# Performance work log

Hardware: AMD Instinct MI355X
Metric: run time of the kernel (lower is better)

## Reference

```python
import jax, jax.numpy as jnp
import numpy as np


def setup_inputs() -> dict:
    key = jax.random.key(0)
    k1, k2 = jax.random.split(key)
    B, Lq, Lc, D = 16, 512, 2048, 1024
    question = jax.random.normal(k1, (B, Lq, D), dtype=jnp.float32)
    context = jax.random.normal(k2, (B, Lc, D), dtype=jnp.float32)
    return {"question": question, "context": context}


def reference(question, context):
    # e = context @ question^T : [B, Lc, Lq]  (unscaled)
    e = jnp.einsum("bcd,bqd->bcq", context, question)
    attn = jax.nn.softmax(e, axis=-1)
    # attention_output = attn @ question : [B, Lc, D]
    attn_out = jnp.einsum("bcq,bqd->bcd", attn, question)
    # concat along feature dim -> [B, Lc, 2D]; dropout is identity at eval
    return jnp.concatenate([context, attn_out], axis=-1)
```

## Files before the change

kernel.cpp:

```cpp
#include <hip/hip_runtime.h>

#define GAS __attribute__((address_space(1)))
#define LAS __attribute__((address_space(3)))

typedef __attribute__((ext_vector_type(8))) _Float16 half8;
typedef __attribute__((ext_vector_type(4))) float floatx4;
typedef __attribute__((ext_vector_type(4))) unsigned short ushort4v;

static constexpr int B_  = 16;
static constexpr int LQ  = 512;
static constexpr int LC  = 2048;
static constexpr int D_  = 1024;
static constexpr int DO  = 2048;
static constexpr int MT  = 64;
static constexpr int BUFSZ = 36864;

__device__ __forceinline__ void gl2lds16(const void* g, void* l) {
  __builtin_amdgcn_global_load_lds((const GAS unsigned int*)g,
                                   (LAS unsigned int*)l, 16, 0, 0);
}

__device__ __forceinline__ unsigned short f2h(float f) {
  return __builtin_bit_cast(unsigned short, (_Float16)f);
}

#define WAITV(a, b)                                                        \
  do {                                                                     \
    if (wave < 4) asm volatile("s_waitcnt vmcnt(" #a ")" ::: "memory");    \
    else          asm volatile("s_waitcnt vmcnt(" #b ")" ::: "memory");    \
  } while (0)

__global__ void qprep_kernel(const float* __restrict__ q,
                             unsigned short* __restrict__ qh,
                             unsigned short* __restrict__ qt) {
  __shared__ unsigned short t[32][33];
  const int b = blockIdx.z, d0 = blockIdx.x * 32, q0 = blockIdx.y * 32;
  const float* src = q + (size_t)b * LQ * D_;
  unsigned short* dq = qh + (size_t)b * LQ * D_;
  unsigned short* dt = qt + (size_t)b * D_ * LQ;
  for (int i = threadIdx.y; i < 32; i += 8) {
    const unsigned short h = f2h(src[(size_t)(q0 + i) * D_ + d0 + threadIdx.x]);
    dq[(size_t)(q0 + i) * D_ + d0 + threadIdx.x] = h;
    t[i][threadIdx.x] = h;
  }
  __syncthreads();
  for (int i = threadIdx.y; i < 32; i += 8)
    dt[(size_t)(d0 + i) * LQ + q0 + threadIdx.x] = t[threadIdx.x][i];
}

__global__ void cprep_kernel(const float* __restrict__ src,
                             unsigned short* __restrict__ dst,
                             float* __restrict__ out) {
  const int nrows = B_ * LC;
  for (int row = blockIdx.x; row < nrows; row += gridDim.x) {
    const float4 v = ((const float4*)(src + (size_t)row * D_))[threadIdx.x];
    ushort4v h;
    h.x = f2h(v.x); h.y = f2h(v.y); h.z = f2h(v.z); h.w = f2h(v.w);
    ((ushort4v*)(dst + (size_t)row * D_))[threadIdx.x] = h;
    ((float4*)(out + (size_t)row * DO))[threadIdx.x] = v;
  }
}

__launch_bounds__(512, 1)
__global__ void attn_main(const unsigned short* __restrict__ qg,
                          const unsigned short* __restrict__ cg,
                          const unsigned short* __restrict__ qtg,
                          unsigned short* __restrict__ pg,
                          float* __restrict__ og) {
  __shared__ __align__(16) char smem[4 * BUFSZ + 2048 + 256];
  float* redf    = (float*)(smem + 4 * BUFSZ);
  float* rowstat = (float*)(smem + 4 * BUFSZ + 2048);

  const int tid  = threadIdx.x;
  const int wave = tid >> 6;
  const int lane = tid & 63;
  const int l15  = lane & 15;
  const int quad = lane >> 4;
  const int q8   = quad * 8;

  const int b    = blockIdx.x & 15;
  const int tile = blockIdx.x >> 4;
  const int c0   = tile * MT;

  const unsigned short* Q  = qg  + (size_t)b * LQ * D_;
  const unsigned short* C  = cg  + (size_t)b * LC * D_;
  const unsigned short* QT = qtg + (size_t)b * D_ * LQ;
  unsigned short*       P  = pg  + (size_t)b * LC * LQ;
  float*                O  = og  + (size_t)b * LC * DO;

  floatx4 acc[4][4];

  auto stage1 = [&](int it, char* buf) {
    const int k0 = it * 32;
#pragma unroll
    for (int j = 0; j < 5; ++j) {
      const int bb = wave + j * 8;
      if (bb < 32) {
        gl2lds16(Q + (size_t)(bb * 16 + l15) * D_ + k0 + q8, buf + bb * 1024);
      } else if (bb < 36) {
        const int mt = bb - 32;
        gl2lds16(C + (size_t)(c0 + mt * 16 + l15) * D_ + k0 + q8,
                 buf + 32768 + mt * 1024);
      }
    }
  };

  auto stage2 = [&](int u, char* buf) {
    const int nh = u >> 4;
    const int kq = (u & 15) * 32;
#pragma unroll
    for (int j = 0; j < 5; ++j) {
      const int bb = wave + j * 8;
      if (bb < 32) {
        gl2lds16(QT + (size_t)(nh * 512 + bb * 16 + l15) * LQ + kq + q8,
                 buf + bb * 1024);
      } else if (bb < 36) {
        const int mt = bb - 32;
        gl2lds16(P + (size_t)(c0 + mt * 16 + l15) * LQ + kq + q8,
                 buf + 32768 + mt * 1024);
      }
    }
  };

  auto compute = [&](const char* buf) {
    half8 af[4], bf[4];
#pragma unroll
    for (int mt = 0; mt < 4; ++mt)
      af[mt] = *(const half8*)(buf + 32768 + mt * 1024 + lane * 16);
#pragma unroll
    for (int nt = 0; nt < 4; ++nt)
      bf[nt] = *(const half8*)(buf + (wave * 4 + nt) * 1024 + lane * 16);
    __builtin_amdgcn_s_setprio(1);
#pragma unroll
    for (int mt = 0; mt < 4; ++mt)
#pragma unroll
      for (int nt = 0; nt < 4; ++nt)
        acc[mt][nt] = __builtin_amdgcn_mfma_f32_16x16x32_f16(
            af[mt], bf[nt], acc[mt][nt], 0, 0, 0);
    __builtin_amdgcn_s_setprio(0);
  };

#pragma unroll
  for (int i = 0; i < 4; ++i)
#pragma unroll
    for (int j = 0; j < 4; ++j) acc[i][j] = floatx4{0.f, 0.f, 0.f, 0.f};

  stage1(0, smem);
  stage1(1, smem + BUFSZ);
  stage1(2, smem + 2 * BUFSZ);
#pragma unroll 1
  for (int t = 0; t < 32; ++t) {
    if (t <= 29)      WAITV(10, 8);
    else if (t == 30) WAITV(5, 4);
    else asm volatile("s_waitcnt vmcnt(0)" ::: "memory");
    __builtin_amdgcn_s_barrier();
    __builtin_amdgcn_sched_barrier(0);
    if (t + 3 < 32) stage1(t + 3, smem + ((t + 3) & 3) * BUFSZ);
    compute(smem + (t & 3) * BUFSZ);
    asm volatile("" ::: "memory");
    __builtin_amdgcn_s_barrier();
  }

#pragma unroll
  for (int mt = 0; mt < 4; ++mt)
#pragma unroll
    for (int r = 0; r < 4; ++r) {
      float m = fmaxf(fmaxf(acc[mt][0][r], acc[mt][1][r]),
                      fmaxf(acc[mt][2][r], acc[mt][3][r]));
      m = fmaxf(m, __shfl_xor(m, 1, 64));
      m = fmaxf(m, __shfl_xor(m, 2, 64));
      m = fmaxf(m, __shfl_xor(m, 4, 64));
      m = fmaxf(m, __shfl_xor(m, 8, 64));
      if (l15 == 0) redf[wave * 64 + mt * 16 + quad * 4 + r] = m;
    }
  __syncthreads();
  if (tid < 64) {
    float m = redf[tid];
#pragma unroll
    for (int w = 1; w < 8; ++w) m = fmaxf(m, redf[w * 64 + tid]);
    rowstat[tid] = m;
  }
  __syncthreads();
#pragma unroll
  for (int mt = 0; mt < 4; ++mt)
#pragma unroll
    for (int r = 0; r < 4; ++r) {
      const float m = rowstat[mt * 16 + quad * 4 + r];
      float s = 0.f;
#pragma unroll
      for (int nt = 0; nt < 4; ++nt) {
        const float e = __expf(acc[mt][nt][r] - m);
        acc[mt][nt][r] = e;
        s += e;
      }
      s += __shfl_xor(s, 1, 64);
      s += __shfl_xor(s, 2, 64);
      s += __shfl_xor(s, 4, 64);
      s += __shfl_xor(s, 8, 64);
      if (l15 == 0) redf[wave * 64 + mt * 16 + quad * 4 + r] = s;
    }
  __syncthreads();
  if (tid < 64) {
    float s = 0.f;
#pragma unroll
    for (int w = 0; w < 8; ++w) s += redf[w * 64 + tid];
    rowstat[tid] = 1.0f / s;
  }
  __syncthreads();
#pragma unroll
  for (int mt = 0; mt < 4; ++mt)
#pragma unroll
    for (int r = 0; r < 4; ++r) {
      const float inv = rowstat[mt * 16 + quad * 4 + r];
      const size_t rowoff =
          (size_t)(c0 + mt * 16 + quad * 4 + r) * LQ + wave * 64 + l15;
#pragma unroll
      for (int nt = 0; nt < 4; ++nt)
        P[rowoff + nt * 16] = f2h(acc[mt][nt][r] * inv);
    }
  asm volatile("s_waitcnt vmcnt(0)" ::: "memory");
  __syncthreads();

  stage2(0, smem);
  stage2(1, smem + BUFSZ);
  stage2(2, smem + 2 * BUFSZ);
#pragma unroll 1
  for (int u = 0; u < 32; ++u) {
    if ((u & 15) == 0) {
#pragma unroll
      for (int i = 0; i < 4; ++i)
#pragma unroll
        for (int j = 0; j < 4; ++j) acc[i][j] = floatx4{0.f, 0.f, 0.f, 0.f};
    }
    if (u <= 29)      WAITV(10, 8);
    else if (u == 30) WAITV(5, 4);
    else asm volatile("s_waitcnt vmcnt(0)" ::: "memory");
    __builtin_amdgcn_s_barrier();
    __builtin_amdgcn_sched_barrier(0);
    if (u + 3 < 32) stage2(u + 3, smem + ((u + 3) & 3) * BUFSZ);
    compute(smem + (u & 3) * BUFSZ);
    asm volatile("" ::: "memory");
    __builtin_amdgcn_s_barrier();
    if ((u & 15) == 15) {
      const int nh = u >> 4;
#pragma unroll
      for (int mt = 0; mt < 4; ++mt)
#pragma unroll
        for (int r = 0; r < 4; ++r) {
          const size_t rowoff = (size_t)(c0 + mt * 16 + quad * 4 + r) * DO +
                                D_ + nh * 512 + wave * 64 + l15;
#pragma unroll
          for (int nt = 0; nt < 4; ++nt)
            O[rowoff + nt * 16] = acc[mt][nt][r];
        }
    }
  }
}

extern "C" void kernel_launch(void* const* d_in, const int* in_sizes, int n_in,
                              void* d_out, int out_size, void* d_ws, size_t ws_size,
                              hipStream_t stream) {
  (void)in_sizes; (void)n_in; (void)out_size; (void)ws_size;
  const float* q = (const float*)d_in[0];
  const float* c = (const float*)d_in[1];
  float* out = (float*)d_out;
  unsigned short* qh  = (unsigned short*)d_ws;
  unsigned short* ch  = qh  + (size_t)B_ * LQ * D_;
  unsigned short* qth = ch  + (size_t)B_ * LC * D_;
  unsigned short* p   = qth + (size_t)B_ * D_ * LQ;
  qprep_kernel<<<dim3(D_ / 32, LQ / 32, B_), dim3(32, 8), 0, stream>>>(q, qh, qth);
  cprep_kernel<<<2048, 256, 0, stream>>>(c, ch, out);
  attn_main<<<dim3(B_ * (LC / MT)), dim3(512), 0, stream>>>(qh, ch, qth, p, out);
}
```

Baseline: 565.8 us.

## Double context tile to 128 rows with three-stage LDS pipeline

```diff
diff --git a/kernel.cpp b/kernel.cpp
--- a/kernel.cpp
+++ b/kernel.cpp
@@ -12,8 +12,8 @@
 static constexpr int LC  = 2048;
 static constexpr int D_  = 1024;
 static constexpr int DO  = 2048;
-static constexpr int MT  = 64;
-static constexpr int BUFSZ = 36864;
+static constexpr int MT  = 128;
+static constexpr int BUFSZ = 40960;
 
 __device__ __forceinline__ void gl2lds16(const void* g, void* l) {
   __builtin_amdgcn_global_load_lds((const GAS unsigned int*)g,
@@ -23,12 +23,6 @@
 __device__ __forceinline__ unsigned short f2h(float f) {
   return __builtin_bit_cast(unsigned short, (_Float16)f);
 }
-
-#define WAITV(a, b)                                                        \
-  do {                                                                     \
-    if (wave < 4) asm volatile("s_waitcnt vmcnt(" #a ")" ::: "memory");    \
-    else          asm volatile("s_waitcnt vmcnt(" #b ")" ::: "memory");    \
-  } while (0)
 
 __global__ void qprep_kernel(const float* __restrict__ q,
                              unsigned short* __restrict__ qh,
@@ -67,9 +61,9 @@
                           const unsigned short* __restrict__ qtg,
                           unsigned short* __restrict__ pg,
                           float* __restrict__ og) {
-  __shared__ __align__(16) char smem[4 * BUFSZ + 2048 + 256];
-  float* redf    = (float*)(smem + 4 * BUFSZ);
-  float* rowstat = (float*)(smem + 4 * BUFSZ + 2048);
+  __shared__ __align__(16) char smem[3 * BUFSZ + 4096 + 512];
+  float* redf    = (float*)(smem + 3 * BUFSZ);
+  float* rowstat = (float*)(smem + 3 * BUFSZ + 4096);
 
   const int tid  = threadIdx.x;
   const int wave = tid >> 6;
@@ -88,7 +82,7 @@
   unsigned short*       P  = pg  + (size_t)b * LC * LQ;
   float*                O  = og  + (size_t)b * LC * DO;
 
-  floatx4 acc[4][4];
+  floatx4 acc[8][4];
 
   auto stage1 = [&](int it, char* buf) {
     const int k0 = it * 32;
@@ -97,7 +91,7 @@
       const int bb = wave + j * 8;
       if (bb < 32) {
         gl2lds16(Q + (size_t)(bb * 16 + l15) * D_ + k0 + q8, buf + bb * 1024);
-      } else if (bb < 36) {
+      } else {
         const int mt = bb - 32;
         gl2lds16(C + (size_t)(c0 + mt * 16 + l15) * D_ + k0 + q8,
                  buf + 32768 + mt * 1024);
@@ -114,7 +108,7 @@
       if (bb < 32) {
         gl2lds16(QT + (size_t)(nh * 512 + bb * 16 + l15) * LQ + kq + q8,
                  buf + bb * 1024);
-      } else if (bb < 36) {
+      } else {
         const int mt = bb - 32;
         gl2lds16(P + (size_t)(c0 + mt * 16 + l15) * LQ + kq + q8,
                  buf + 32768 + mt * 1024);
@@ -123,46 +117,48 @@
   };
 
   auto compute = [&](const char* buf) {
-    half8 af[4], bf[4];
-#pragma unroll
-    for (int mt = 0; mt < 4; ++mt)
-      af[mt] = *(const half8*)(buf + 32768 + mt * 1024 + lane * 16);
+    half8 bf[4];
 #pragma unroll
     for (int nt = 0; nt < 4; ++nt)
       bf[nt] = *(const half8*)(buf + (wave * 4 + nt) * 1024 + lane * 16);
     __builtin_amdgcn_s_setprio(1);
 #pragma unroll
-    for (int mt = 0; mt < 4; ++mt)
+    for (int mt = 0; mt < 8; ++mt) {
+      const half8 a = *(const half8*)(buf + 32768 + mt * 1024 + lane * 16);
 #pragma unroll
       for (int nt = 0; nt < 4; ++nt)
         acc[mt][nt] = __builtin_amdgcn_mfma_f32_16x16x32_f16(
-            af[mt], bf[nt], acc[mt][nt], 0, 0, 0);
+            a, bf[nt], acc[mt][nt], 0, 0, 0);
+    }
     __builtin_amdgcn_s_setprio(0);
   };
 
 #pragma unroll
-  for (int i = 0; i < 4; ++i)
+  for (int i = 0; i < 8; ++i)
 #pragma unroll
     for (int j = 0; j < 4; ++j) acc[i][j] = floatx4{0.f, 0.f, 0.f, 0.f};
 
   stage1(0, smem);
   stage1(1, smem + BUFSZ);
-  stage1(2, smem + 2 * BUFSZ);
+  int cur = 0;
 #pragma unroll 1
   for (int t = 0; t < 32; ++t) {
-    if (t <= 29)      WAITV(10, 8);
-    else if (t == 30) WAITV(5, 4);
-    else asm volatile("s_waitcnt vmcnt(0)" ::: "memory");
+    if (t < 31) asm volatile("s_waitcnt vmcnt(5)" ::: "memory");
+    else        asm volatile("s_waitcnt vmcnt(0)" ::: "memory");
     __builtin_amdgcn_s_barrier();
     __builtin_amdgcn_sched_barrier(0);
-    if (t + 3 < 32) stage1(t + 3, smem + ((t + 3) & 3) * BUFSZ);
-    compute(smem + (t & 3) * BUFSZ);
+    if (t + 2 < 32) {
+      int s2 = cur + 2; if (s2 >= 3) s2 -= 3;
+      stage1(t + 2, smem + s2 * BUFSZ);
+    }
+    compute(smem + cur * BUFSZ);
     asm volatile("" ::: "memory");
     __builtin_amdgcn_s_barrier();
-  }
-
-#pragma unroll
-  for (int mt = 0; mt < 4; ++mt)
+    if (++cur == 3) cur = 0;
+  }
+
+#pragma unroll
+  for (int mt = 0; mt < 8; ++mt)
 #pragma unroll
     for (int r = 0; r < 4; ++r) {
       float m = fmaxf(fmaxf(acc[mt][0][r], acc[mt][1][r]),
@@ -171,18 +167,18 @@
       m = fmaxf(m, __shfl_xor(m, 2, 64));
       m = fmaxf(m, __shfl_xor(m, 4, 64));
       m = fmaxf(m, __shfl_xor(m, 8, 64));
-      if (l15 == 0) redf[wave * 64 + mt * 16 + quad * 4 + r] = m;
-    }
-  __syncthreads();
-  if (tid < 64) {
+      if (l15 == 0) redf[wave * 128 + mt * 16 + quad * 4 + r] = m;
+    }
+  __syncthreads();
+  if (tid < 128) {
     float m = redf[tid];
 #pragma unroll
-    for (int w = 1; w < 8; ++w) m = fmaxf(m, redf[w * 64 + tid]);
+    for (int w = 1; w < 8; ++w) m = fmaxf(m, redf[w * 128 + tid]);
     rowstat[tid] = m;
   }
   __syncthreads();
 #pragma unroll
-  for (int mt = 0; mt < 4; ++mt)
+  for (int mt = 0; mt < 8; ++mt)
 #pragma unroll
     for (int r = 0; r < 4; ++r) {
       const float m = rowstat[mt * 16 + quad * 4 + r];
@@ -197,18 +193,18 @@
       s += __shfl_xor(s, 2, 64);
       s += __shfl_xor(s, 4, 64);
       s += __shfl_xor(s, 8, 64);
-      if (l15 == 0) redf[wave * 64 + mt * 16 + quad * 4 + r] = s;
-    }
-  __syncthreads();
-  if (tid < 64) {
+      if (l15 == 0) redf[wave * 128 + mt * 16 + quad * 4 + r] = s;
+    }
+  __syncthreads();
+  if (tid < 128) {
     float s = 0.f;
 #pragma unroll
-    for (int w = 0; w < 8; ++w) s += redf[w * 64 + tid];
+    for (int w = 0; w < 8; ++w) s += redf[w * 128 + tid];
     rowstat[tid] = 1.0f / s;
   }
   __syncthreads();
 #pragma unroll
-  for (int mt = 0; mt < 4; ++mt)
+  for (int mt = 0; mt < 8; ++mt)
 #pragma unroll
     for (int r = 0; r < 4; ++r) {
       const float inv = rowstat[mt * 16 + quad * 4 + r];
@@ -223,28 +219,31 @@
 
   stage2(0, smem);
   stage2(1, smem + BUFSZ);
-  stage2(2, smem + 2 * BUFSZ);
+  cur = 0;
 #pragma unroll 1
   for (int u = 0; u < 32; ++u) {
     if ((u & 15) == 0) {
 #pragma unroll
-      for (int i = 0; i < 4; ++i)
+      for (int i = 0; i < 8; ++i)
 #pragma unroll
         for (int j = 0; j < 4; ++j) acc[i][j] = floatx4{0.f, 0.f, 0.f, 0.f};
     }
-    if (u <= 29)      WAITV(10, 8);
-    else if (u == 30) WAITV(5, 4);
-    else asm volatile("s_waitcnt vmcnt(0)" ::: "memory");
+    if (u < 31) asm volatile("s_waitcnt vmcnt(5)" ::: "memory");
+    else        asm volatile("s_waitcnt vmcnt(0)" ::: "memory");
     __builtin_amdgcn_s_barrier();
     __builtin_amdgcn_sched_barrier(0);
-    if (u + 3 < 32) stage2(u + 3, smem + ((u + 3) & 3) * BUFSZ);
-    compute(smem + (u & 3) * BUFSZ);
+    if (u + 2 < 32) {
+      int s2 = cur + 2; if (s2 >= 3) s2 -= 3;
+      stage2(u + 2, smem + s2 * BUFSZ);
+    }
+    compute(smem + cur * BUFSZ);
     asm volatile("" ::: "memory");
     __builtin_amdgcn_s_barrier();
+    if (++cur == 3) cur = 0;
     if ((u & 15) == 15) {
       const int nh = u >> 4;
 #pragma unroll
-      for (int mt = 0; mt < 4; ++mt)
+      for (int mt = 0; mt < 8; ++mt)
 #pragma unroll
         for (int r = 0; r < 4; ++r) {
           const size_t rowoff = (size_t)(c0 + mt * 16 + quad * 4 + r) * DO +
```

After: 516.7 us. 1.09x faster.
